# Kernel tuning notes

Hardware: AMD Instinct MI355X
Metric: run time of the kernel (lower is better)

## Reference

```python
import jax, jax.numpy as jnp
import numpy as np

B = 65536
NQ = 8
NL = 3
FEAT = 64 * 3 * 3 + NQ  # 584


def _conv(x, w, b):
    # x: (B,C,H,W), w: (O,I,3,3), padding=1 -> SAME
    y = jax.lax.conv_general_dilated(
        x, w, window_strides=(1, 1), padding='SAME',
        dimension_numbers=('NCHW', 'OIHW', 'NCHW'))
    return y + b[None, :, None, None]


def _maxpool2(x):
    return jax.lax.reduce_window(
        x, -jnp.inf, jax.lax.max, (1, 1, 2, 2), (1, 1, 2, 2), 'VALID')


def _quantum_sim(x, qp):
    # x: (B,NQ); qp: (NL,NQ,3). Within a layer, qubit q depends only on its own
    # previous state (tanh term), so vectorize over qubits and scan over layers.
    x_next = jnp.roll(x, -1, axis=1)  # x[:, (q+1) % NQ]

    def step(q_state, rot):  # rot: (NQ,3)
        new = jnp.sin(rot[:, 0] * x) * jnp.cos(rot[:, 1] * x_next) \
              + jnp.tanh(rot[:, 2] * q_state)
        return new, None

    q0 = jnp.zeros_like(x)
    qf, _ = jax.lax.scan(step, q0, qp)
    return qf


def setup_inputs() -> dict:
    key = jax.random.key(0)
    ks = jax.random.split(key, 16)

    def w(k, shape, fan_in):
        lim = 1.0 / np.sqrt(fan_in)
        return jax.random.uniform(k, shape, jnp.float32, -lim, lim)

    return {
        'board_state': jax.random.normal(ks[0], (B, 3, 6, 6), jnp.float32),
        'target_positions': jax.random.randint(ks[1], (4, 2), 0, 6).astype(jnp.int64),
        'conv1_w': w(ks[2], (16, 3, 3, 3), 3 * 9), 'conv1_b': w(ks[3], (16,), 3 * 9),
        'conv2_w': w(ks[4], (32, 16, 3, 3), 16 * 9), 'conv2_b': w(ks[5], (32,), 16 * 9),
        'conv3_w': w(ks[6], (64, 32, 3, 3), 32 * 9), 'conv3_b': w(ks[7], (64,), 32 * 9),
        'quantum_params': jax.random.normal(ks[8], (NL, NQ, 3), jnp.float32),
        'pt_w1': w(ks[9], (FEAT, 128), FEAT), 'pt_b1': w(ks[9], (128,), FEAT),
        'pt_w2': w(ks[10], (128, 64), 128), 'pt_b2': w(ks[10], (64,), 128),
        'pt_w3': w(ks[11], (64, 2), 64), 'pt_b3': w(ks[11], (2,), 64),
        'cf_w1': w(ks[12], (FEAT, 64), FEAT), 'cf_b1': w(ks[12], (64,), FEAT),
        'cf_w2': w(ks[13], (64, 1), 64), 'cf_b2': w(ks[13], (1,), 64),
    }


def reference(board_state, target_positions,
              conv1_w, conv1_b, conv2_w, conv2_b, conv3_w, conv3_b,
              quantum_params,
              pt_w1, pt_b1, pt_w2, pt_b2, pt_w3, pt_b3,
              cf_w1, cf_b1, cf_w2, cf_b2):
    b = board_state.shape[0]
    h = jax.nn.relu(_conv(board_state, conv1_w, conv1_b))   # (B,16,6,6)
    h = jax.nn.relu(_conv(h, conv2_w, conv2_b))             # (B,32,6,6)
    h = _maxpool2(h)                                        # (B,32,3,3)
    h = jax.nn.relu(_conv(h, conv3_w, conv3_b))             # (B,64,3,3)
    conv_flat = h.reshape(b, -1)                            # (B,576)

    board_flat = board_state.reshape(b, -1)
    q_feat = _quantum_sim(board_flat[:, :NQ], quantum_params)  # (B,NQ)

    feats = jnp.concatenate([conv_flat, q_feat], axis=1)    # (B,584)

    # piece-type head (Dropout is identity in eval)
    t = jax.nn.relu(feats @ pt_w1 + pt_b1)
    t = jax.nn.relu(t @ pt_w2 + pt_b2)
    type_logits = t @ pt_w3 + pt_b3
    type_probs = jax.nn.softmax(type_logits, axis=1)        # (B,2)

    # confidence head
    c = jax.nn.relu(feats @ cf_w1 + cf_b1)
    confidence = jax.nn.sigmoid(c @ cf_w2 + cf_b2)          # (B,1)

    # target_positions never affect the math (pos_encoding unused in torch source);
    # the same probs/confidence are reported for every position.
    return jnp.concatenate([type_probs, confidence], axis=1)  # (B,3)
```

## Files before the change

### kernel.cpp

```cpp
#include <hip/hip_runtime.h>

typedef _Float16 h8 __attribute__((ext_vector_type(8)));
typedef _Float16 h4 __attribute__((ext_vector_type(4)));
typedef float f32x4 __attribute__((ext_vector_type(4)));

union HU { _Float16 h; unsigned short u; };
__device__ __forceinline__ unsigned short f2h(float f) { HU x; x.h = (_Float16)f; return x.u; }
__device__ __forceinline__ float h2f(unsigned short u) { HU x; x.u = u; return (float)x.h; }

#define MFMA16(a, b, c) __builtin_amdgcn_mfma_f32_16x16x32_f16((a), (b), (c), 0, 0, 0)

__global__ void k_prep(const float* __restrict__ w1, const float* __restrict__ w2,
                       const float* __restrict__ w3,
                       const float* __restrict__ ptw1, const float* __restrict__ cfw1,
                       const float* __restrict__ ptw2, const float* __restrict__ ptw3,
                       const float* __restrict__ cfw2,
                       unsigned short* __restrict__ w1f,
                       unsigned short* __restrict__ w2f,
                       unsigned short* __restrict__ w3f,
                       unsigned short* __restrict__ w1hd,
                       unsigned short* __restrict__ w2hd,
                       unsigned short* __restrict__ w3hd) {
    int gid = blockIdx.x * 256 + threadIdx.x;
    int gs = gridDim.x * 256;
    for (int e = gid; e < 1024; e += gs) {
        int f = e >> 9, lane = (e >> 3) & 63, j = e & 7;
        int k = ((lane >> 4) << 3) + j, oc = lane & 15;
        int r, within;
        if (f == 0) { r = k >> 4; within = k & 15; }
        else        { r = 2;      within = k; }
        int tx = within >> 2, ch = within & 3;
        float v = 0.f;
        if (tx < 3 && ch < 3) v = w1[oc * 27 + ch * 9 + r * 3 + tx];
        w1f[e] = f2h(v);
    }
    for (int e = gid; e < 9216; e += gs) {
        int j = e & 7, lane = (e >> 3) & 63, fo = e >> 9;
        int ot = fo & 1, t = fo >> 1;
        int k = ((lane >> 4) * 8) + j, oc = ot * 16 + (lane & 15);
        float v = (k < 16) ? w2[oc * 144 + k * 9 + t] : 0.f;
        w2f[e] = f2h(v);
    }
    for (int e = gid; e < 18432; e += gs) {
        int j = e & 7, lane = (e >> 3) & 63, fo = e >> 9;
        int oti = fo & 1, t = (fo >> 1) % 9, otp = (fo >> 1) / 9;
        int ic = ((lane >> 4) * 8) + j, oc = (otp * 2 + oti) * 16 + (lane & 15);
        w3f[e] = f2h(w3[oc * 288 + ic * 9 + t]);
    }
    for (int s = gid; s < 608 * 192; s += gs) {
        int k = s / 192, n = s - k * 192;
        float v = 0.f;
        if (k < 584) {
            int f = (k < 576) ? ((k & 63) * 9 + (k >> 6)) : k;
            v = (n < 128) ? ptw1[f * 128 + n] : cfw1[f * 64 + (n - 128)];
        }
        int kk = k >> 5, hi = (k & 31) >> 3, j = k & 7, nt = n >> 4;
        int e = (((kk * 12 + nt) << 6) | (hi << 4) | (n & 15)) << 3 | j;
        w1hd[e] = f2h(v);
    }
    for (int s = gid; s < 8192; s += gs) {
        int k = s >> 6, n = s & 63;
        float v = ptw2[k * 64 + n];
        int kk = k >> 5, hi = (k & 31) >> 3, j = k & 7, nt = n >> 4;
        int e = ((((kk << 2) | nt) << 6) | (hi << 4) | (n & 15)) << 3 | j;
        w2hd[e] = f2h(v);
    }
    for (int e = gid; e < 2048; e += gs) {
        int j = e & 7, lane = (e >> 3) & 63, kk = e >> 9;
        int k = kk * 32 + ((lane >> 4) * 8) + j, n = lane & 15;
        float v = 0.f;
        if (k < 64) { if (n < 2) v = ptw3[k * 2 + n]; }
        else        { if (n == 2) v = cfw2[k - 64]; }
        w3hd[e] = f2h(v);
    }
}

#define BDS4 260
#define BDH4 (16 * BDS4)
#define A1S 584
#define A2S 296
#define FTS 616
#define HSH 200
#define RA_OFF 19712
#define O_OFF 26112
#define LDSTOT 26368

__global__ __launch_bounds__(256, 3) void k_fused(
    const float* __restrict__ board,
    const float* __restrict__ b1, const float* __restrict__ b2,
    const float* __restrict__ b3, const float* __restrict__ qp,
    const unsigned short* __restrict__ w1f,
    const unsigned short* __restrict__ w2f,
    const unsigned short* __restrict__ w3f,
    const unsigned short* __restrict__ w1hd,
    const unsigned short* __restrict__ w2hd,
    const unsigned short* __restrict__ w3hd,
    const float* __restrict__ ptb1, const float* __restrict__ ptb2,
    const float* __restrict__ ptb3, const float* __restrict__ cfb1,
    const float* __restrict__ cfb2,
    float* __restrict__ out)
{
    __shared__ __align__(16) unsigned short LDSH[LDSTOT];
    const int tid = threadIdx.x, wid = tid >> 6, lane = tid & 63;
    const int g = wid >> 1, w2 = wid & 1;
    const int col = lane & 15, q = lane >> 4;
    const long long gg0 = (long long)blockIdx.x * 32;
    const f32x4 ZERO4 = {0.f, 0.f, 0.f, 0.f};

    unsigned short* A1 = LDSH + g * 9856;
    unsigned short* A2 = A1;
    unsigned short* Hb = LDSH + RA_OFF;
    float* O = (float*)(LDSH + O_OFF);

    for (int e = tid; e < BDH4 / 4; e += 256)
        ((unsigned long long*)(LDSH + RA_OFF))[e] = 0ULL;
    __syncthreads();

    float qv[2];
    h8 w1r0 = ((const h8*)w1f)[lane];
    h8 w1r1 = ((const h8*)w1f)[64 + lane];
    float b1v = b1[col];
    #pragma unroll
    for (int gi = 0; gi < 2; gi++) {
        for (int e = tid; e < 16 * 108; e += 256) {
            int ss = e / 108, r2 = e % 108, ch = r2 / 36, p = r2 % 36;
            float v = board[(gg0 + gi * 16) * 108 + e];
            LDSH[RA_OFF + ss * BDS4 + ((p / 6 + 1) * 8 + (p % 6) + 1) * 4 + ch] =
                f2h(v);
        }
        __syncthreads();
        if (tid < 128) {
            int ss = tid >> 3, qq = tid & 7;
            int base = RA_OFF + ss * BDS4;
            int p8a = ((qq / 6 + 1) * 8 + (qq % 6) + 1) * 4;
            int e2 = (qq + 1) & 7;
            int p8b = ((e2 / 6 + 1) * 8 + (e2 % 6) + 1) * 4;
            float xq = h2f(LDSH[base + p8a]);
            float xn = h2f(LDSH[base + p8b]);
            float st = 0.f;
            for (int l = 0; l < 3; l++) {
                float a0 = qp[l * 24 + qq * 3], a1 = qp[l * 24 + qq * 3 + 1],
                      a2 = qp[l * 24 + qq * 3 + 2];
                st = sinf(a0 * xq) * cosf(a1 * xn) + tanhf(a2 * st);
            }
            qv[gi] = st;
        }
        {
            unsigned short* A1g = LDSH + gi * 9856;
            const int bs = RA_OFF + col * BDS4;
            const int rsel = q >> 1, wo = (q & 1) * 8;
            for (int p = wid * 9; p < wid * 9 + 9; p++) {
                int y = p / 6, x = p % 6;
                int ab1 = bs + ((y + rsel) * 8 + x) * 4 + wo;
                int ab2 = bs + ((y + 2) * 8 + x) * 4 + wo;
                union { h8 v; h4 h[2]; } a1v, a2v;
                a1v.h[0] = *(const h4*)&LDSH[ab1];
                a1v.h[1] = *(const h4*)&LDSH[ab1 + 4];
                a2v.h[0] = *(const h4*)&LDSH[ab2];
                a2v.h[1] = *(const h4*)&LDSH[ab2 + 4];
                f32x4 c = MFMA16(a1v.v, w1r0, ZERO4);
                c = MFMA16(a2v.v, w1r1, c);
                #pragma unroll
                for (int r = 0; r < 4; r++)
                    A1g[(q * 4 + r) * A1S + p * 16 + col] =
                        f2h(fmaxf(c[r] + b1v, 0.f));
            }
        }
        __syncthreads();
    }

    f32x4 pooled2[9];
    #pragma unroll
    for (int pp = 0; pp < 9; pp++) pooled2[pp] = ZERO4;
    {
        h8 W2r[9];
        #pragma unroll
        for (int t = 0; t < 9; t++)
            W2r[t] = ((const h8*)w2f)[(t * 2 + w2) * 64 + lane];
        float b2v = b2[w2 * 16 + col];
        const int sA1 = col * A1S;
        const int kho = (q & 1) * 8;

        h8 R[3][6];
        #pragma unroll
        for (int x = 0; x < 6; x++) {
            R[0][x] = *(const h8*)&A1[sA1 + (0 * 6 + x) * 16 + kho];
            R[1][x] = *(const h8*)&A1[sA1 + (1 * 6 + x) * 16 + kho];
        }
        #pragma unroll
        for (int y = 0; y < 6; y++) {
            if (y >= 1 && y <= 4) {
                const int nr = y + 1, slot = nr % 3;
                #pragma unroll
                for (int x = 0; x < 6; x++)
                    R[slot][x] = *(const h8*)&A1[sA1 + (nr * 6 + x) * 16 + kho];
            }
            f32x4 acc[6];
            #pragma unroll
            for (int x = 0; x < 6; x++) acc[x] = ZERO4;
            #pragma unroll
            for (int dy = -1; dy <= 1; dy++) {
                const int ry = y + dy;
                if (ry < 0 || ry > 5) continue;
                const int slot = ry % 3;
                #pragma unroll
                for (int x = 0; x < 6; x++)
                    #pragma unroll
                    for (int dx = -1; dx <= 1; dx++) {
                        const int sx = x + dx;
                        if (sx < 0 || sx > 5) continue;
                        acc[x] = MFMA16(R[slot][sx],
                                        W2r[(dy + 1) * 3 + (dx + 1)], acc[x]);
                    }
            }
            const int pr = y >> 1;
            #pragma unroll
            for (int px = 0; px < 3; px++)
                #pragma unroll
                for (int xx = 0; xx < 2; xx++)
                    #pragma unroll
                    for (int r = 0; r < 4; r++)
                        pooled2[pr * 3 + px][r] =
                            fmaxf(pooled2[pr * 3 + px][r],
                                  acc[px * 2 + xx][r] + b2v);
        }
    }
    __syncthreads();
    #pragma unroll
    for (int pp = 0; pp < 9; pp++)
        #pragma unroll
        for (int r = 0; r < 4; r++)
            A2[(q * 4 + r) * A2S + pp * 32 + w2 * 16 + col] =
                f2h(pooled2[pp][r]);
    __syncthreads();

    f32x4 c3a[9], c3b[9];
    {
        const int otp = w2;
        const int sA2 = col * A2S;
        h8 W3r[18];
        #pragma unroll
        for (int f = 0; f < 18; f++)
            W3r[f] = ((const h8*)w3f)[(otp * 18 + f) * 64 + lane];
        #pragma unroll
        for (int p = 0; p < 9; p++) {
            const int y = p / 3, x = p % 3;
            f32x4 acc0 = ZERO4, acc1 = ZERO4;
            #pragma unroll
            for (int t = 0; t < 9; t++) {
                const int sy = y + t / 3 - 1, sx = x + t % 3 - 1;
                if (sy < 0 || sy >= 3 || sx < 0 || sx >= 3) continue;
                h8 a = *(const h8*)&A2[sA2 + (sy * 3 + sx) * 32 + q * 8];
                acc0 = MFMA16(a, W3r[t * 2 + 0], acc0);
                acc1 = MFMA16(a, W3r[t * 2 + 1], acc1);
            }
            c3a[p] = acc0; c3b[p] = acc1;
        }
    }
    __syncthreads();

    {
        const int otp = w2;
        float b3v0 = b3[(otp * 2 + 0) * 16 + col];
        float b3v1 = b3[(otp * 2 + 1) * 16 + col];
        int oc0 = (otp * 2 + 0) * 16 + col, oc1 = (otp * 2 + 1) * 16 + col;
        #pragma unroll
        for (int p = 0; p < 9; p++)
            #pragma unroll
            for (int r = 0; r < 4; r++) {
                int row = g * 16 + q * 4 + r;
                LDSH[row * FTS + p * 64 + oc0] = f2h(fmaxf(c3a[p][r] + b3v0, 0.f));
                LDSH[row * FTS + p * 64 + oc1] = f2h(fmaxf(c3b[p][r] + b3v1, 0.f));
            }
        if (tid < 128) {
            int ss = tid >> 3, qq = tid & 7;
            LDSH[ss * FTS + 576 + qq] = f2h(qv[0]);
            LDSH[(ss + 16) * FTS + 576 + qq] = f2h(qv[1]);
        }
        for (int e = tid; e < 1024; e += 256)
            LDSH[(e >> 5) * FTS + 584 + (e & 31)] = 0;
    }
    __syncthreads();

    {
        f32x4 acc[2][3];
        #pragma unroll
        for (int mt = 0; mt < 2; mt++)
            #pragma unroll
            for (int nt = 0; nt < 3; nt++) acc[mt][nt] = ZERO4;
        const h8* wp1 = (const h8*)w1hd;
        const int ntb = wid * 3;
        for (int kk = 0; kk < 19; kk++) {
            h8 a0 = *(const h8*)&LDSH[col * FTS + kk * 32 + q * 8];
            h8 a1 = *(const h8*)&LDSH[(16 + col) * FTS + kk * 32 + q * 8];
            h8 b[3];
            #pragma unroll
            for (int nt = 0; nt < 3; nt++)
                b[nt] = wp1[(kk * 12 + ntb + nt) * 64 + lane];
            #pragma unroll
            for (int nt = 0; nt < 3; nt++) {
                acc[0][nt] = MFMA16(a0, b[nt], acc[0][nt]);
                acc[1][nt] = MFMA16(a1, b[nt], acc[1][nt]);
            }
        }
        #pragma unroll
        for (int nt = 0; nt < 3; nt++) {
            int ntg = ntb + nt;
            float bv = (ntg < 8) ? ptb1[ntg * 16 + col] : cfb1[(ntg - 8) * 16 + col];
            #pragma unroll
            for (int mt = 0; mt < 2; mt++)
                #pragma unroll
                for (int r = 0; r < 4; r++)
                    Hb[(mt * 16 + q * 4 + r) * HSH + ntg * 16 + col] =
                        f2h(fmaxf(acc[mt][nt][r] + bv, 0.f));
        }
    }
    __syncthreads();

    {
        f32x4 acc2[2];
        acc2[0] = ZERO4; acc2[1] = ZERO4;
        const h8* wp2 = (const h8*)w2hd;
        const int nt2 = wid;
        #pragma unroll
        for (int kk = 0; kk < 4; kk++) {
            h8 a0 = *(const h8*)&Hb[col * HSH + kk * 32 + q * 8];
            h8 a1 = *(const h8*)&Hb[(16 + col) * HSH + kk * 32 + q * 8];
            h8 b = wp2[(kk * 4 + nt2) * 64 + lane];
            acc2[0] = MFMA16(a0, b, acc2[0]);
            acc2[1] = MFMA16(a1, b, acc2[1]);
        }
        __syncthreads();
        float bv2 = ptb2[nt2 * 16 + col];
        #pragma unroll
        for (int mt = 0; mt < 2; mt++)
            #pragma unroll
            for (int r = 0; r < 4; r++)
                Hb[(mt * 16 + q * 4 + r) * HSH + nt2 * 16 + col] =
                    f2h(fmaxf(acc2[mt][r] + bv2, 0.f));
    }
    __syncthreads();

    if (wid < 2) {
        const int mt = wid;
        f32x4 a3 = ZERO4;
        #pragma unroll
        for (int kk = 0; kk < 4; kk++) {
            int base = (kk < 2) ? kk * 32 : kk * 32 + 64;
            h8 a = *(const h8*)&Hb[(mt * 16 + col) * HSH + base + q * 8];
            h8 b = ((const h8*)w3hd)[kk * 64 + lane];
            a3 = MFMA16(a, b, a3);
        }
        if (col < 3) {
            float bv = (col < 2) ? ptb3[col] : cfb2[0];
            #pragma unroll
            for (int r = 0; r < 4; r++)
                O[(mt * 16 + q * 4 + r) * 4 + col] = a3[r] + bv;
        }
        if (lane < 16) {
            int s = mt * 16 + lane;
            float l0 = O[s * 4 + 0], l1 = O[s * 4 + 1], l2 = O[s * 4 + 2];
            float m = fmaxf(l0, l1);
            float e0 = expf(l0 - m), e1 = expf(l1 - m);
            float inv = 1.f / (e0 + e1);
            float* op = out + (gg0 + s) * 3;
            op[0] = e0 * inv;
            op[1] = e1 * inv;
            op[2] = 1.f / (1.f + expf(-l2));
        }
    }
}

extern "C" void kernel_launch(void* const* d_in, const int* in_sizes, int n_in,
                              void* d_out, int out_size, void* d_ws, size_t ws_size,
                              hipStream_t stream) {
    const float* board = (const float*)d_in[0];
    const float* c1w  = (const float*)d_in[2];
    const float* c1b  = (const float*)d_in[3];
    const float* c2w  = (const float*)d_in[4];
    const float* c2b  = (const float*)d_in[5];
    const float* c3w  = (const float*)d_in[6];
    const float* c3b  = (const float*)d_in[7];
    const float* qp   = (const float*)d_in[8];
    const float* ptw1 = (const float*)d_in[9];
    const float* ptb1 = (const float*)d_in[10];
    const float* ptw2 = (const float*)d_in[11];
    const float* ptb2 = (const float*)d_in[12];
    const float* ptw3 = (const float*)d_in[13];
    const float* ptb3 = (const float*)d_in[14];
    const float* cfw1 = (const float*)d_in[15];
    const float* cfb1 = (const float*)d_in[16];
    const float* cfw2 = (const float*)d_in[17];
    const float* cfb2 = (const float*)d_in[18];
    float* out = (float*)d_out;

    int Btot = in_sizes[0] / 108;

    unsigned short* w1f   = (unsigned short*)d_ws;
    unsigned short* w2f   = (unsigned short*)((char*)d_ws + 2048);
    unsigned short* w3f   = (unsigned short*)((char*)d_ws + 20480);
    unsigned short* w1hd  = (unsigned short*)((char*)d_ws + 57344);
    unsigned short* w2hd  = (unsigned short*)((char*)d_ws + 290816);
    unsigned short* w3hd  = (unsigned short*)((char*)d_ws + 307200);

    hipLaunchKernelGGL(k_prep, dim3(256), dim3(256), 0, stream,
                       c1w, c2w, c3w, ptw1, cfw1, ptw2, ptw3, cfw2,
                       w1f, w2f, w3f, w1hd, w2hd, w3hd);
    hipLaunchKernelGGL(k_fused, dim3(Btot / 32), dim3(256), 0, stream,
                       board, c1b, c2b, c3b, qp, w1f, w2f, w3f,
                       w1hd, w2hd, w3hd, ptb1, ptb2, ptb3, cfb1, cfb2, out);
}
```

Baseline: 174.3 us.

## Halve samples per block and split conv stages across waves for occupancy

Each block now handles 16 samples instead of 32. The conv2 and conv3 stages are split so waves divide output rows and positions, instead of each wave pair owning one 16-sample group. LDS use roughly halves and launch bounds rise from 3 to 6 blocks per CU, trading per-block work for more resident waves. Fast-math sin, cos and exp intrinsics replace the precise versions, which slightly changes numerics, and weight register loads are now repeated across twice as many blocks.

```diff
diff --git a/kernel.cpp b/kernel.cpp
--- a/kernel.cpp
+++ b/kernel.cpp
@@ -75,17 +75,73 @@
     }
 }
 
-#define BDS4 260
-#define BDH4 (16 * BDS4)
 #define A1S 584
 #define A2S 296
 #define FTS 616
+#define BDS4 260
+#define BD_OFF 9344
+#define H_OFF 9856
 #define HSH 200
-#define RA_OFF 19712
-#define O_OFF 26112
-#define LDSTOT 26368
-
-__global__ __launch_bounds__(256, 3) void k_fused(
+#define O_OFF 13056
+#define LDSTOT 13504
+
+template<int OT, int Y0, int Y1>
+__device__ __forceinline__ void conv2_sweep(
+    const unsigned short* LDSH, const h8* W2r, float b2v,
+    int q, int col, f32x4* pooled2)
+{
+    const f32x4 ZERO4 = {0.f, 0.f, 0.f, 0.f};
+    const int sA1 = col * A1S;
+    const int kho = (q & 1) * 8;
+    h8 R[3][6];
+    #pragma unroll
+    for (int y = Y0; y <= Y1; y++) {
+        if (y == Y0) {
+            #pragma unroll
+            for (int rr = Y0 - 1; rr <= Y0 + 1; rr++)
+                if (rr >= 0 && rr <= 5) {
+                    #pragma unroll
+                    for (int x = 0; x < 6; x++)
+                        R[rr % 3][x] =
+                            *(const h8*)&LDSH[sA1 + (rr * 6 + x) * 16 + kho];
+                }
+        } else if (y + 1 <= 5) {
+            #pragma unroll
+            for (int x = 0; x < 6; x++)
+                R[(y + 1) % 3][x] =
+                    *(const h8*)&LDSH[sA1 + ((y + 1) * 6 + x) * 16 + kho];
+        }
+        f32x4 acc[6];
+        #pragma unroll
+        for (int x = 0; x < 6; x++) acc[x] = ZERO4;
+        #pragma unroll
+        for (int dy = -1; dy <= 1; dy++) {
+            const int ry = y + dy;
+            if (ry < 0 || ry > 5) continue;
+            const int slot = ry % 3;
+            #pragma unroll
+            for (int x = 0; x < 6; x++)
+                #pragma unroll
+                for (int dx = -1; dx <= 1; dx++) {
+                    const int sx = x + dx;
+                    if (sx < 0 || sx > 5) continue;
+                    acc[x] = MFMA16(R[slot][sx],
+                                    W2r[(dy + 1) * 3 + (dx + 1)], acc[x]);
+                }
+        }
+        const int pi = (y >> 1) - (Y0 >> 1);
+        #pragma unroll
+        for (int px = 0; px < 3; px++)
+            #pragma unroll
+            for (int xx = 0; xx < 2; xx++)
+                #pragma unroll
+                for (int r = 0; r < 4; r++)
+                    pooled2[pi * 3 + px][r] =
+                        fmaxf(pooled2[pi * 3 + px][r], acc[px * 2 + xx][r] + b2v);
+    }
+}
+
+__global__ __launch_bounds__(256, 6) void k_fused(
     const float* __restrict__ board,
     const float* __restrict__ b1, const float* __restrict__ b2,
     const float* __restrict__ b3, const float* __restrict__ qp,
@@ -102,252 +158,197 @@
 {
     __shared__ __align__(16) unsigned short LDSH[LDSTOT];
     const int tid = threadIdx.x, wid = tid >> 6, lane = tid & 63;
-    const int g = wid >> 1, w2 = wid & 1;
     const int col = lane & 15, q = lane >> 4;
-    const long long gg0 = (long long)blockIdx.x * 32;
+    const long long gg0 = (long long)blockIdx.x * 16;
     const f32x4 ZERO4 = {0.f, 0.f, 0.f, 0.f};
-
-    unsigned short* A1 = LDSH + g * 9856;
-    unsigned short* A2 = A1;
-    unsigned short* Hb = LDSH + RA_OFF;
+    unsigned short* Hb = LDSH + H_OFF;
     float* O = (float*)(LDSH + O_OFF);
 
-    for (int e = tid; e < BDH4 / 4; e += 256)
-        ((unsigned long long*)(LDSH + RA_OFF))[e] = 0ULL;
-    __syncthreads();
-
-    float qv[2];
-    h8 w1r0 = ((const h8*)w1f)[lane];
-    h8 w1r1 = ((const h8*)w1f)[64 + lane];
-    float b1v = b1[col];
+    for (int e = tid; e < 1040; e += 256)
+        ((unsigned long long*)LDSH)[2336 + e] = 0ULL;
+    __syncthreads();
+
+    for (int e = tid; e < 16 * 108; e += 256) {
+        int ss = e / 108, r2 = e % 108, ch = r2 / 36, p = r2 % 36;
+        float v = board[gg0 * 108 + e];
+        LDSH[BD_OFF + ss * BDS4 + ((p / 6 + 1) * 8 + (p % 6) + 1) * 4 + ch] =
+            f2h(v);
+    }
+    __syncthreads();
+
+    float qv = 0.f;
+    if (tid < 128) {
+        int ss = tid >> 3, qq = tid & 7;
+        int base = BD_OFF + ss * BDS4;
+        int p8a = ((qq / 6 + 1) * 8 + (qq % 6) + 1) * 4;
+        int e2 = (qq + 1) & 7;
+        int p8b = ((e2 / 6 + 1) * 8 + (e2 % 6) + 1) * 4;
+        float xq = h2f(LDSH[base + p8a]);
+        float xn = h2f(LDSH[base + p8b]);
+        float st = 0.f;
+        for (int l = 0; l < 3; l++) {
+            float a0 = qp[l * 24 + qq * 3], a1 = qp[l * 24 + qq * 3 + 1],
+                  a2 = qp[l * 24 + qq * 3 + 2];
+            st = __sinf(a0 * xq) * __cosf(a1 * xn) + tanhf(a2 * st);
+        }
+        qv = st;
+    }
+
+    {
+        h8 w1r0 = ((const h8*)w1f)[lane];
+        h8 w1r1 = ((const h8*)w1f)[64 + lane];
+        float b1v = b1[col];
+        const int bs = BD_OFF + col * BDS4;
+        const int rsel = q >> 1, wo = (q & 1) * 8;
+        for (int p = wid * 9; p < wid * 9 + 9; p++) {
+            int y = p / 6, x = p % 6;
+            int ab1 = bs + ((y + rsel) * 8 + x) * 4 + wo;
+            int ab2 = bs + ((y + 2) * 8 + x) * 4 + wo;
+            union { h8 v; h4 h[2]; } a1v, a2v;
+            a1v.h[0] = *(const h4*)&LDSH[ab1];
+            a1v.h[1] = *(const h4*)&LDSH[ab1 + 4];
+            a2v.h[0] = *(const h4*)&LDSH[ab2];
+            a2v.h[1] = *(const h4*)&LDSH[ab2 + 4];
+            f32x4 c = MFMA16(a1v.v, w1r0, ZERO4);
+            c = MFMA16(a2v.v, w1r1, c);
+            #pragma unroll
+            for (int r = 0; r < 4; r++)
+                LDSH[(q * 4 + r) * A1S + p * 16 + col] =
+                    f2h(fmaxf(c[r] + b1v, 0.f));
+        }
+    }
+    __syncthreads();
+
+    const int ot = wid & 1, yh = wid >> 1;
+    f32x4 pooled2[6];
     #pragma unroll
-    for (int gi = 0; gi < 2; gi++) {
-        for (int e = tid; e < 16 * 108; e += 256) {
-            int ss = e / 108, r2 = e % 108, ch = r2 / 36, p = r2 % 36;
-            float v = board[(gg0 + gi * 16) * 108 + e];
-            LDSH[RA_OFF + ss * BDS4 + ((p / 6 + 1) * 8 + (p % 6) + 1) * 4 + ch] =
-                f2h(v);
-        }
-        __syncthreads();
-        if (tid < 128) {
-            int ss = tid >> 3, qq = tid & 7;
-            int base = RA_OFF + ss * BDS4;
-            int p8a = ((qq / 6 + 1) * 8 + (qq % 6) + 1) * 4;
-            int e2 = (qq + 1) & 7;
-            int p8b = ((e2 / 6 + 1) * 8 + (e2 % 6) + 1) * 4;
-            float xq = h2f(LDSH[base + p8a]);
-            float xn = h2f(LDSH[base + p8b]);
-            float st = 0.f;
-            for (int l = 0; l < 3; l++) {
-                float a0 = qp[l * 24 + qq * 3], a1 = qp[l * 24 + qq * 3 + 1],
-                      a2 = qp[l * 24 + qq * 3 + 2];
-                st = sinf(a0 * xq) * cosf(a1 * xn) + tanhf(a2 * st);
-            }
-            qv[gi] = st;
-        }
-        {
-            unsigned short* A1g = LDSH + gi * 9856;
-            const int bs = RA_OFF + col * BDS4;
-            const int rsel = q >> 1, wo = (q & 1) * 8;
-            for (int p = wid * 9; p < wid * 9 + 9; p++) {
-                int y = p / 6, x = p % 6;
-                int ab1 = bs + ((y + rsel) * 8 + x) * 4 + wo;
-                int ab2 = bs + ((y + 2) * 8 + x) * 4 + wo;
-                union { h8 v; h4 h[2]; } a1v, a2v;
-                a1v.h[0] = *(const h4*)&LDSH[ab1];
-                a1v.h[1] = *(const h4*)&LDSH[ab1 + 4];
-                a2v.h[0] = *(const h4*)&LDSH[ab2];
-                a2v.h[1] = *(const h4*)&LDSH[ab2 + 4];
-                f32x4 c = MFMA16(a1v.v, w1r0, ZERO4);
-                c = MFMA16(a2v.v, w1r1, c);
+    for (int i = 0; i < 6; i++) pooled2[i] = ZERO4;
+    {
+        h8 W2r[9];
+        #pragma unroll
+        for (int t = 0; t < 9; t++)
+            W2r[t] = ((const h8*)w2f)[(t * 2 + ot) * 64 + lane];
+        float b2v = b2[ot * 16 + col];
+        if (yh == 0) conv2_sweep<0, 0, 3>(LDSH, W2r, b2v, q, col, pooled2);
+        else         conv2_sweep<1, 4, 5>(LDSH, W2r, b2v, q, col, pooled2);
+    }
+    __syncthreads();
+    {
+        const int pr0 = (yh == 0) ? 0 : 2, npr = (yh == 0) ? 2 : 1;
+        for (int pi = 0; pi < npr; pi++)
+            #pragma unroll
+            for (int px = 0; px < 3; px++)
                 #pragma unroll
                 for (int r = 0; r < 4; r++)
-                    A1g[(q * 4 + r) * A1S + p * 16 + col] =
-                        f2h(fmaxf(c[r] + b1v, 0.f));
-            }
-        }
-        __syncthreads();
-    }
-
-    f32x4 pooled2[9];
-    #pragma unroll
-    for (int pp = 0; pp < 9; pp++) pooled2[pp] = ZERO4;
-    {
-        h8 W2r[9];
-        #pragma unroll
-        for (int t = 0; t < 9; t++)
-            W2r[t] = ((const h8*)w2f)[(t * 2 + w2) * 64 + lane];
-        float b2v = b2[w2 * 16 + col];
-        const int sA1 = col * A1S;
-        const int kho = (q & 1) * 8;
-
-        h8 R[3][6];
-        #pragma unroll
-        for (int x = 0; x < 6; x++) {
-            R[0][x] = *(const h8*)&A1[sA1 + (0 * 6 + x) * 16 + kho];
-            R[1][x] = *(const h8*)&A1[sA1 + (1 * 6 + x) * 16 + kho];
-        }
-        #pragma unroll
-        for (int y = 0; y < 6; y++) {
-            if (y >= 1 && y <= 4) {
-                const int nr = y + 1, slot = nr % 3;
-                #pragma unroll
-                for (int x = 0; x < 6; x++)
-                    R[slot][x] = *(const h8*)&A1[sA1 + (nr * 6 + x) * 16 + kho];
-            }
-            f32x4 acc[6];
-            #pragma unroll
-            for (int x = 0; x < 6; x++) acc[x] = ZERO4;
-            #pragma unroll
-            for (int dy = -1; dy <= 1; dy++) {
-                const int ry = y + dy;
-                if (ry < 0 || ry > 5) continue;
-                const int slot = ry % 3;
-                #pragma unroll
-                for (int x = 0; x < 6; x++)
-                    #pragma unroll
-                    for (int dx = -1; dx <= 1; dx++) {
-                        const int sx = x + dx;
-                        if (sx < 0 || sx > 5) continue;
-                        acc[x] = MFMA16(R[slot][sx],
-                                        W2r[(dy + 1) * 3 + (dx + 1)], acc[x]);
-                    }
-            }
-            const int pr = y >> 1;
-            #pragma unroll
-            for (int px = 0; px < 3; px++)
-                #pragma unroll
-                for (int xx = 0; xx < 2; xx++)
-                    #pragma unroll
-                    for (int r = 0; r < 4; r++)
-                        pooled2[pr * 3 + px][r] =
-                            fmaxf(pooled2[pr * 3 + px][r],
-                                  acc[px * 2 + xx][r] + b2v);
-        }
-    }
-    __syncthreads();
-    #pragma unroll
-    for (int pp = 0; pp < 9; pp++)
-        #pragma unroll
-        for (int r = 0; r < 4; r++)
-            A2[(q * 4 + r) * A2S + pp * 32 + w2 * 16 + col] =
-                f2h(pooled2[pp][r]);
-    __syncthreads();
-
-    f32x4 c3a[9], c3b[9];
-    {
-        const int otp = w2;
+                    LDSH[(q * 4 + r) * A2S + ((pr0 + pi) * 3 + px) * 32 +
+                         ot * 16 + col] = f2h(pooled2[pi * 3 + px][r]);
+    }
+    __syncthreads();
+
+    const int otp = wid & 1, ph = wid >> 1;
+    const int P0 = ph ? 5 : 0, NP3 = ph ? 4 : 5;
+    f32x4 c3a[5], c3b[5];
+    {
         const int sA2 = col * A2S;
         h8 W3r[18];
         #pragma unroll
         for (int f = 0; f < 18; f++)
             W3r[f] = ((const h8*)w3f)[(otp * 18 + f) * 64 + lane];
-        #pragma unroll
-        for (int p = 0; p < 9; p++) {
+        for (int pi = 0; pi < 5; pi++) {
+            if (pi >= NP3) break;
+            const int p = P0 + pi;
             const int y = p / 3, x = p % 3;
             f32x4 acc0 = ZERO4, acc1 = ZERO4;
             #pragma unroll
             for (int t = 0; t < 9; t++) {
                 const int sy = y + t / 3 - 1, sx = x + t % 3 - 1;
                 if (sy < 0 || sy >= 3 || sx < 0 || sx >= 3) continue;
-                h8 a = *(const h8*)&A2[sA2 + (sy * 3 + sx) * 32 + q * 8];
+                h8 a = *(const h8*)&LDSH[sA2 + (sy * 3 + sx) * 32 + q * 8];
                 acc0 = MFMA16(a, W3r[t * 2 + 0], acc0);
                 acc1 = MFMA16(a, W3r[t * 2 + 1], acc1);
             }
-            c3a[p] = acc0; c3b[p] = acc1;
-        }
-    }
-    __syncthreads();
-
-    {
-        const int otp = w2;
+            c3a[pi] = acc0; c3b[pi] = acc1;
+        }
+    }
+    __syncthreads();
+
+    {
         float b3v0 = b3[(otp * 2 + 0) * 16 + col];
         float b3v1 = b3[(otp * 2 + 1) * 16 + col];
         int oc0 = (otp * 2 + 0) * 16 + col, oc1 = (otp * 2 + 1) * 16 + col;
-        #pragma unroll
-        for (int p = 0; p < 9; p++)
+        for (int pi = 0; pi < 5; pi++) {
+            if (pi >= NP3) break;
+            const int p = P0 + pi;
             #pragma unroll
             for (int r = 0; r < 4; r++) {
-                int row = g * 16 + q * 4 + r;
-                LDSH[row * FTS + p * 64 + oc0] = f2h(fmaxf(c3a[p][r] + b3v0, 0.f));
-                LDSH[row * FTS + p * 64 + oc1] = f2h(fmaxf(c3b[p][r] + b3v1, 0.f));
+                int row = q * 4 + r;
+                LDSH[row * FTS + p * 64 + oc0] =
+                    f2h(fmaxf(c3a[pi][r] + b3v0, 0.f));
+                LDSH[row * FTS + p * 64 + oc1] =
+                    f2h(fmaxf(c3b[pi][r] + b3v1, 0.f));
             }
+        }
         if (tid < 128) {
             int ss = tid >> 3, qq = tid & 7;
-            LDSH[ss * FTS + 576 + qq] = f2h(qv[0]);
-            LDSH[(ss + 16) * FTS + 576 + qq] = f2h(qv[1]);
-        }
-        for (int e = tid; e < 1024; e += 256)
+            LDSH[ss * FTS + 576 + qq] = f2h(qv);
+        }
+        for (int e = tid; e < 512; e += 256)
             LDSH[(e >> 5) * FTS + 584 + (e & 31)] = 0;
     }
     __syncthreads();
 
     {
-        f32x4 acc[2][3];
-        #pragma unroll
-        for (int mt = 0; mt < 2; mt++)
-            #pragma unroll
-            for (int nt = 0; nt < 3; nt++) acc[mt][nt] = ZERO4;
+        f32x4 acc[3];
+        #pragma unroll
+        for (int nt = 0; nt < 3; nt++) acc[nt] = ZERO4;
         const h8* wp1 = (const h8*)w1hd;
         const int ntb = wid * 3;
         for (int kk = 0; kk < 19; kk++) {
             h8 a0 = *(const h8*)&LDSH[col * FTS + kk * 32 + q * 8];
-            h8 a1 = *(const h8*)&LDSH[(16 + col) * FTS + kk * 32 + q * 8];
             h8 b[3];
             #pragma unroll
             for (int nt = 0; nt < 3; nt++)
                 b[nt] = wp1[(kk * 12 + ntb + nt) * 64 + lane];
             #pragma unroll
-            for (int nt = 0; nt < 3; nt++) {
-                acc[0][nt] = MFMA16(a0, b[nt], acc[0][nt]);
-                acc[1][nt] = MFMA16(a1, b[nt], acc[1][nt]);
-            }
+            for (int nt = 0; nt < 3; nt++)
+                acc[nt] = MFMA16(a0, b[nt], acc[nt]);
         }
         #pragma unroll
         for (int nt = 0; nt < 3; nt++) {
             int ntg = ntb + nt;
             float bv = (ntg < 8) ? ptb1[ntg * 16 + col] : cfb1[(ntg - 8) * 16 + col];
             #pragma unroll
-            for (int mt = 0; mt < 2; mt++)
-                #pragma unroll
-                for (int r = 0; r < 4; r++)
-                    Hb[(mt * 16 + q * 4 + r) * HSH + ntg * 16 + col] =
-                        f2h(fmaxf(acc[mt][nt][r] + bv, 0.f));
-        }
-    }
-    __syncthreads();
-
-    {
-        f32x4 acc2[2];
-        acc2[0] = ZERO4; acc2[1] = ZERO4;
+            for (int r = 0; r < 4; r++)
+                Hb[(q * 4 + r) * HSH + ntg * 16 + col] =
+                    f2h(fmaxf(acc[nt][r] + bv, 0.f));
+        }
+    }
+    __syncthreads();
+
+    {
+        f32x4 acc2 = ZERO4;
         const h8* wp2 = (const h8*)w2hd;
-        const int nt2 = wid;
         #pragma unroll
         for (int kk = 0; kk < 4; kk++) {
-            h8 a0 = *(const h8*)&Hb[col * HSH + kk * 32 + q * 8];
-            h8 a1 = *(const h8*)&Hb[(16 + col) * HSH + kk * 32 + q * 8];
-            h8 b = wp2[(kk * 4 + nt2) * 64 + lane];
-            acc2[0] = MFMA16(a0, b, acc2[0]);
-            acc2[1] = MFMA16(a1, b, acc2[1]);
+            h8 a = *(const h8*)&Hb[col * HSH + kk * 32 + q * 8];
+            h8 b = wp2[(kk * 4 + wid) * 64 + lane];
+            acc2 = MFMA16(a, b, acc2);
         }
         __syncthreads();
-        float bv2 = ptb2[nt2 * 16 + col];
-        #pragma unroll
-        for (int mt = 0; mt < 2; mt++)
-            #pragma unroll
-            for (int r = 0; r < 4; r++)
-                Hb[(mt * 16 + q * 4 + r) * HSH + nt2 * 16 + col] =
-                    f2h(fmaxf(acc2[mt][r] + bv2, 0.f));
-    }
-    __syncthreads();
-
-    if (wid < 2) {
-        const int mt = wid;
+        float bv2 = ptb2[wid * 16 + col];
+        #pragma unroll
+        for (int r = 0; r < 4; r++)
+            Hb[(q * 4 + r) * HSH + wid * 16 + col] =
+                f2h(fmaxf(acc2[r] + bv2, 0.f));
+    }
+    __syncthreads();
+
+    if (wid == 0) {
         f32x4 a3 = ZERO4;
         #pragma unroll
         for (int kk = 0; kk < 4; kk++) {
             int base = (kk < 2) ? kk * 32 : kk * 32 + 64;
-            h8 a = *(const h8*)&Hb[(mt * 16 + col) * HSH + base + q * 8];
+            h8 a = *(const h8*)&Hb[col * HSH + base + q * 8];
             h8 b = ((const h8*)w3hd)[kk * 64 + lane];
             a3 = MFMA16(a, b, a3);
         }
@@ -355,18 +356,17 @@
             float bv = (col < 2) ? ptb3[col] : cfb2[0];
             #pragma unroll
             for (int r = 0; r < 4; r++)
-                O[(mt * 16 + q * 4 + r) * 4 + col] = a3[r] + bv;
+                O[(q * 4 + r) * 4 + col] = a3[r] + bv;
         }
         if (lane < 16) {
-            int s = mt * 16 + lane;
-            float l0 = O[s * 4 + 0], l1 = O[s * 4 + 1], l2 = O[s * 4 + 2];
+            float l0 = O[lane * 4 + 0], l1 = O[lane * 4 + 1], l2 = O[lane * 4 + 2];
             float m = fmaxf(l0, l1);
-            float e0 = expf(l0 - m), e1 = expf(l1 - m);
+            float e0 = __expf(l0 - m), e1 = __expf(l1 - m);
             float inv = 1.f / (e0 + e1);
-            float* op = out + (gg0 + s) * 3;
+            float* op = out + (gg0 + lane) * 3;
             op[0] = e0 * inv;
             op[1] = e1 * inv;
-            op[2] = 1.f / (1.f + expf(-l2));
+            op[2] = 1.f / (1.f + __expf(-l2));
         }
     }
 }
@@ -406,7 +406,7 @@
     hipLaunchKernelGGL(k_prep, dim3(256), dim3(256), 0, stream,
                        c1w, c2w, c3w, ptw1, cfw1, ptw2, ptw3, cfw2,
                        w1f, w2f, w3f, w1hd, w2hd, w3hd);
-    hipLaunchKernelGGL(k_fused, dim3(Btot / 32), dim3(256), 0, stream,
+    hipLaunchKernelGGL(k_fused, dim3(Btot / 16), dim3(256), 0, stream,
                        board, c1b, c2b, c3b, qp, w1f, w2f, w3f,
                        w1hd, w2hd, w3hd, ptb1, ptb2, ptb3, cfb1, cfb2, out);
 }
```

After: 479.9 us. 2.75x slower.
